# Kernel tuning notes

Hardware: AMD Instinct MI355X
Metric: run time of the kernel (lower is better)

## Reference

```python
import jax, jax.numpy as jnp
import numpy as np


def setup_inputs() -> dict:
    key = jax.random.key(0)
    k1, k2 = jax.random.split(key)
    B, C, N = 8, 3, 4096
    ori_pcs = jax.random.normal(k1, (B, C, N), dtype=jnp.float32)
    adv_pcs = jax.random.normal(k2, (B, C, N), dtype=jnp.float32)
    return {"ori_pcs": ori_pcs, "adv_pcs": adv_pcs}


def _chamfer(ori_pcs, adv_pcs, single=False, reduce="max"):
    # [B, 3, N] -> [B, N, 3]
    x = jnp.swapaxes(ori_pcs, 1, 2)
    y = jnp.swapaxes(adv_pcs, 1, 2)
    x2 = jnp.sum(x * x, axis=-1)  # [B, N]
    y2 = jnp.sum(y * y, axis=-1)  # [B, M]
    # squared pairwise distances [B, N, M]
    d = x2[:, :, None] + y2[:, None, :] - 2.0 * jnp.einsum("bnd,bmd->bnm", x, y)
    d = jnp.maximum(d, 0.0)
    d1 = jnp.mean(jnp.min(d, axis=2), axis=1)  # ori -> adv, per batch [B]
    if single:
        return jnp.mean(d1)
    d2 = jnp.mean(jnp.min(d, axis=1), axis=1)  # adv -> ori, per batch [B]
    if reduce == "max":
        per_batch = jnp.maximum(d1, d2)
    else:  # 'sum' / 'mean' style fallback
        per_batch = d1 + d2
    return jnp.mean(per_batch)


def reference(ori_pcs, adv_pcs):
    return _chamfer(ori_pcs, adv_pcs, single=False, reduce="max")
```

## Files before the change

### kernel.cpp

```cpp
#include <hip/hip_runtime.h>
#include <float.h>

#define BATCH 8
#define NPTS 4096
#define BLK 512
#define THALF 1024
#define NH 4
#define NRG 8

typedef __attribute__((ext_vector_type(8))) short short8;
typedef __attribute__((ext_vector_type(16))) float floatx16;

union U4S8 { uint4 u; short8 s; };

__device__ inline unsigned short f2bf(float f) {
    unsigned u = __float_as_uint(f);
    return (unsigned short)((u + 0x7FFFu + ((u >> 16) & 1u)) >> 16);
}
__device__ inline float bf2f(unsigned short h) {
    return __uint_as_float(((unsigned)h) << 16);
}
__device__ inline unsigned flag_token(int i) {
    return 0x9E3779B9u * (unsigned)(i + 7);
}

__global__ __launch_bounds__(BLK, 4) void chamfer_partial(
        const float* __restrict__ ori, const float* __restrict__ adv,
        float* __restrict__ rfin) {
    __shared__ uint4 sm[THALF];

    int bx = blockIdx.x;
    int half = bx & (NH - 1);
    int rowgroup = (bx >> 2) & (NRG - 1);
    int dirb = bx >> 5;
    int b = dirb & 7;
    int dir = dirb >> 3;

    const float* qsrc = dir ? adv : ori;
    const float* tsrc = dir ? ori : adv;

    {
        const float* tx = tsrc + (b * 3 + 0) * NPTS;
        const float* ty = tsrc + (b * 3 + 1) * NPTS;
        const float* tz = tsrc + (b * 3 + 2) * NPTS;
        #pragma unroll
        for (int i = 0; i < THALF / BLK; ++i) {
            int p = threadIdx.x + i * BLK;
            int m = half * THALF + p;
            float x = tx[m], y = ty[m], z = tz[m];
            float n2 = fmaf(x, x, fmaf(y, y, z * z));
            unsigned short hx = f2bf(x), hy = f2bf(y), hz = f2bf(z);
            unsigned short lx = f2bf(x - bf2f(hx));
            unsigned short ly = f2bf(y - bf2f(hy));
            unsigned short lz = f2bf(z - bf2f(hz));
            unsigned short h2 = f2bf(n2);
            unsigned short l2 = f2bf(n2 - bf2f(h2));
            uint4 u;
            u.x = (unsigned)hx | ((unsigned)hy << 16);
            u.y = (unsigned)hz | ((unsigned)lx << 16);
            u.z = (unsigned)ly | ((unsigned)lz << 16);
            u.w = (unsigned)h2 | ((unsigned)l2 << 16);
            sm[p] = u;
        }
    }

    int w = threadIdx.x >> 6;
    int l = threadIdx.x & 63;
    int lrow = l & 31;
    int kh = l >> 5;

    short8 afrag0, afrag1;
    #pragma unroll
    for (int bi = 0; bi < 2; ++bi) {
        int q = rowgroup * 512 + (w * 2 + bi) * 32 + lrow;
        float x = qsrc[(b * 3 + 0) * NPTS + q];
        float y = qsrc[(b * 3 + 1) * NPTS + q];
        float z = qsrc[(b * 3 + 2) * NPTS + q];
        float n2 = fmaf(x, x, fmaf(y, y, z * z));
        unsigned short hx = f2bf(x), hy = f2bf(y), hz = f2bf(z);
        unsigned short lx = f2bf(x - bf2f(hx));
        unsigned short ly = f2bf(y - bf2f(hy));
        unsigned short lz = f2bf(z - bf2f(hz));
        unsigned short h2 = f2bf(n2);
        unsigned short l2 = f2bf(n2 - bf2f(h2));
        unsigned short mhx = f2bf(-2.0f * bf2f(hx));
        unsigned short mhy = f2bf(-2.0f * bf2f(hy));
        unsigned short mhz = f2bf(-2.0f * bf2f(hz));
        unsigned short mlx = f2bf(-2.0f * bf2f(lx));
        unsigned short mly = f2bf(-2.0f * bf2f(ly));
        unsigned short mlz = f2bf(-2.0f * bf2f(lz));
        const unsigned short one = 0x3F80;
        union { unsigned short us[8]; short8 s8; } A;
        if (kh == 0) {
            A.us[0] = mhx; A.us[1] = mhy; A.us[2] = mhz;
            A.us[3] = mhx; A.us[4] = mhy; A.us[5] = mhz;
            A.us[6] = one; A.us[7] = one;
        } else {
            A.us[0] = mlx; A.us[1] = mly; A.us[2] = mlz;
            A.us[3] = h2;  A.us[4] = l2;
            A.us[5] = 0;   A.us[6] = 0;   A.us[7] = 0;
        }
        if (bi == 0) afrag0 = A.s8; else afrag1 = A.s8;
    }
    __syncthreads();

    floatx16 zero, rmn0, rmn1;
    #pragma unroll
    for (int r = 0; r < 16; ++r) { zero[r] = 0.0f; rmn0[r] = FLT_MAX; rmn1[r] = FLT_MAX; }

    bool hi = (kh == 1);
    int col = lrow;

    {
        uint4 r0 = sm[col], r1 = sm[32 + col];
        #pragma unroll 1
        for (int ct = 0; ct < 32; ct += 2) {
            U4S8 f0, f1;
            f0.u.x = r0.x;
            f0.u.y = hi ? ((r0.y & 0xFFFFu) | 0x3F800000u) : r0.y;
            f0.u.z = hi ? 0x00003F80u : r0.z;
            f0.u.w = hi ? 0u : r0.w;
            f1.u.x = r1.x;
            f1.u.y = hi ? ((r1.y & 0xFFFFu) | 0x3F800000u) : r1.y;
            f1.u.z = hi ? 0x00003F80u : r1.z;
            f1.u.w = hi ? 0u : r1.w;
            int nt = (ct + 2) & 31;
            r0 = sm[(nt << 5) + col];
            r1 = sm[((nt + 1) << 5) + col];
            {
                floatx16 a0 = __builtin_amdgcn_mfma_f32_32x32x16_bf16(afrag0, f0.s, zero, 0, 0, 0);
                floatx16 a1 = __builtin_amdgcn_mfma_f32_32x32x16_bf16(afrag0, f1.s, zero, 0, 0, 0);
                #pragma unroll
                for (int r = 0; r < 16; ++r)
                    rmn0[r] = fminf(fminf(rmn0[r], a0[r]), a1[r]);
            }
            {
                floatx16 c0 = __builtin_amdgcn_mfma_f32_32x32x16_bf16(afrag1, f0.s, zero, 0, 0, 0);
                floatx16 c1 = __builtin_amdgcn_mfma_f32_32x32x16_bf16(afrag1, f1.s, zero, 0, 0, 0);
                #pragma unroll
                for (int r = 0; r < 16; ++r)
                    rmn1[r] = fminf(fminf(rmn1[r], c0[r]), c1[r]);
            }
        }
    }

    bool b0 = (l & 1), b1 = (l & 2), b2 = (l & 4), b3 = (l & 8);

#define FOLD(v)                                                                \
    {                                                                          \
        _Pragma("unroll")                                                      \
        for (int i = 0; i < 8; ++i) {                                          \
            float send = b0 ? v[i] : v[i + 8];                                 \
            float recv = __shfl_xor(send, 1);                                  \
            v[i] = fminf(b0 ? v[i + 8] : v[i], recv);                          \
        }                                                                      \
        _Pragma("unroll")                                                      \
        for (int i = 0; i < 4; ++i) {                                          \
            float send = b1 ? v[i] : v[i + 4];                                 \
            float recv = __shfl_xor(send, 2);                                  \
            v[i] = fminf(b1 ? v[i + 4] : v[i], recv);                          \
        }                                                                      \
        _Pragma("unroll")                                                      \
        for (int i = 0; i < 2; ++i) {                                          \
            float send = b2 ? v[i] : v[i + 2];                                 \
            float recv = __shfl_xor(send, 4);                                  \
            v[i] = fminf(b2 ? v[i + 2] : v[i], recv);                          \
        }                                                                      \
        {                                                                      \
            float send = b3 ? v[0] : v[1];                                     \
            float recv = __shfl_xor(send, 8);                                  \
            v[0] = fminf(b3 ? v[1] : v[0], recv);                              \
        }                                                                      \
        v[0] = fminf(v[0], __shfl_xor(v[0], 16));                              \
    }

    FOLD(rmn0);
    FOLD(rmn1);
#undef FOLD

    if ((l & 16) == 0) {
        int g = l & 15;
        int rr = ((g & 1) << 3) | ((g & 2) << 1) | ((g & 4) >> 1) | ((g & 8) >> 3);
        int rowin = (rr & 3) + 8 * (rr >> 2) + 4 * kh;
        float* base = rfin + (((size_t)(dirb * NH + half)) << 12)
                    + rowgroup * 512;
        base[(w * 2 + 0) * 32 + rowin] = rmn0[0];
        base[(w * 2 + 1) * 32 + rowin] = rmn1[0];
    }
}

__global__ __launch_bounds__(256) void combine_kernel(
        const float* __restrict__ rfin, float* __restrict__ bsum,
        unsigned* __restrict__ flags, float* __restrict__ out) {
    __shared__ float ws[4];
    __shared__ float sh[16];
    int dirb = blockIdx.x;
    const float* p = rfin + (((size_t)dirb * NH) << 12);
    float s = 0.0f;
    #pragma unroll
    for (int k = 0; k < 16; ++k) {
        int row = k * 256 + threadIdx.x;
        float m = fminf(fminf(p[row], p[(1 << 12) + row]),
                        fminf(p[(2 << 12) + row], p[(3 << 12) + row]));
        s += fmaxf(m, 0.0f);
    }
    for (int off = 32; off > 0; off >>= 1) s += __shfl_down(s, off);
    int wid = threadIdx.x >> 6, lane = threadIdx.x & 63;
    if (lane == 0) ws[wid] = s;
    __syncthreads();
    if (threadIdx.x == 0) {
        float t = ws[0] + ws[1] + ws[2] + ws[3];
        atomicExch((unsigned*)(bsum + dirb), __float_as_uint(t));
        __threadfence();
        atomicExch(flags + dirb, flag_token(dirb));
    }

    if (dirb == 0) {
        __syncthreads();
        int t = threadIdx.x;
        if (t < 16) {
            unsigned want = flag_token(t);
            while (atomicAdd(flags + t, 0u) != want) {
                __builtin_amdgcn_s_sleep(1);
            }
            sh[t] = __uint_as_float(atomicAdd((unsigned*)(bsum + t), 0u));
        }
        __syncthreads();
        if (t == 0) {
            float acc = 0.0f;
            #pragma unroll
            for (int bb = 0; bb < BATCH; ++bb)
                acc += fmaxf(sh[bb], sh[8 + bb]);
            out[0] = acc * (1.0f / (float)NPTS) * (1.0f / (float)BATCH);
        }
    }
}

extern "C" void kernel_launch(void* const* d_in, const int* in_sizes, int n_in,
                              void* d_out, int out_size, void* d_ws, size_t ws_size,
                              hipStream_t stream) {
    const float* ori = (const float*)d_in[0];
    const float* adv = (const float*)d_in[1];
    float* out = (float*)d_out;

    float* rfin = (float*)d_ws;
    float* bsum = rfin + (size_t)16 * NH * NPTS;
    unsigned* flags = (unsigned*)(bsum + 16);

    chamfer_partial<<<16 * NRG * NH, BLK, 0, stream>>>(ori, adv, rfin);
    combine_kernel<<<16, 256, 0, stream>>>(rfin, bsum, flags, out);
}
```

Baseline: 19.47 us.

## Precompute B fragments in LDS, software-pipeline MFMA loop, widen combine grid

Stores both the low-half and high-half B fragment variants in shared memory so the inner loop no longer selects and masks fragment words per iteration. The MFMA loop is software-pipelined so one set of min-reductions overlaps the next MFMA pair, with loads issued a step ahead. The combine kernel is split into 64 blocks, each summing a quarter of the rows, and a final block folds the partial sums. This doubles LDS per block and adds more flag spinning in the combine stage.

```diff
diff --git a/kernel.cpp b/kernel.cpp
--- a/kernel.cpp
+++ b/kernel.cpp
@@ -12,6 +12,7 @@
 typedef __attribute__((ext_vector_type(16))) float floatx16;
 
 union U4S8 { uint4 u; short8 s; };
+__device__ inline short8 asS8(uint4 u) { U4S8 t; t.u = u; return t.s; }
 
 __device__ inline unsigned short f2bf(float f) {
     unsigned u = __float_as_uint(f);
@@ -27,7 +28,7 @@
 __global__ __launch_bounds__(BLK, 4) void chamfer_partial(
         const float* __restrict__ ori, const float* __restrict__ adv,
         float* __restrict__ rfin) {
-    __shared__ uint4 sm[THALF];
+    __shared__ uint4 fr[2 * THALF];
 
     int bx = blockIdx.x;
     int half = bx & (NH - 1);
@@ -55,12 +56,18 @@
             unsigned short lz = f2bf(z - bf2f(hz));
             unsigned short h2 = f2bf(n2);
             unsigned short l2 = f2bf(n2 - bf2f(h2));
-            uint4 u;
-            u.x = (unsigned)hx | ((unsigned)hy << 16);
-            u.y = (unsigned)hz | ((unsigned)lx << 16);
-            u.z = (unsigned)ly | ((unsigned)lz << 16);
-            u.w = (unsigned)h2 | ((unsigned)l2 << 16);
-            sm[p] = u;
+            uint4 v0;
+            v0.x = (unsigned)hx | ((unsigned)hy << 16);
+            v0.y = (unsigned)hz | ((unsigned)lx << 16);
+            v0.z = (unsigned)ly | ((unsigned)lz << 16);
+            v0.w = (unsigned)h2 | ((unsigned)l2 << 16);
+            uint4 v1;
+            v1.x = v0.x;
+            v1.y = (unsigned)hz | (0x3F80u << 16);
+            v1.z = 0x00003F80u;
+            v1.w = 0u;
+            fr[p] = v0;
+            fr[THALF + p] = v1;
         }
     }
 
@@ -108,40 +115,39 @@
     #pragma unroll
     for (int r = 0; r < 16; ++r) { zero[r] = 0.0f; rmn0[r] = FLT_MAX; rmn1[r] = FLT_MAX; }
 
-    bool hi = (kh == 1);
-    int col = lrow;
+    const uint4* tp = fr + kh * THALF + lrow;
 
     {
-        uint4 r0 = sm[col], r1 = sm[32 + col];
+        uint4 f0 = tp[0], f1 = tp[1 << 5];
+        floatx16 a0 = __builtin_amdgcn_mfma_f32_32x32x16_bf16(afrag0, asS8(f0), zero, 0, 0, 0);
+        floatx16 a1 = __builtin_amdgcn_mfma_f32_32x32x16_bf16(afrag0, asS8(f1), zero, 0, 0, 0);
+        uint4 fn0 = tp[2 << 5], fn1 = tp[3 << 5];
+        #pragma unroll
+        for (int r = 0; r < 16; ++r)
+            rmn0[r] = fminf(fminf(rmn0[r], a0[r]), a1[r]);
+        floatx16 c0 = __builtin_amdgcn_mfma_f32_32x32x16_bf16(afrag1, asS8(f0), zero, 0, 0, 0);
+        floatx16 c1 = __builtin_amdgcn_mfma_f32_32x32x16_bf16(afrag1, asS8(f1), zero, 0, 0, 0);
+        f0 = fn0; f1 = fn1;
+
         #pragma unroll 1
-        for (int ct = 0; ct < 32; ct += 2) {
-            U4S8 f0, f1;
-            f0.u.x = r0.x;
-            f0.u.y = hi ? ((r0.y & 0xFFFFu) | 0x3F800000u) : r0.y;
-            f0.u.z = hi ? 0x00003F80u : r0.z;
-            f0.u.w = hi ? 0u : r0.w;
-            f1.u.x = r1.x;
-            f1.u.y = hi ? ((r1.y & 0xFFFFu) | 0x3F800000u) : r1.y;
-            f1.u.z = hi ? 0x00003F80u : r1.z;
-            f1.u.w = hi ? 0u : r1.w;
+        for (int ct = 2; ct < 32; ct += 2) {
+            #pragma unroll
+            for (int r = 0; r < 16; ++r)
+                rmn1[r] = fminf(fminf(rmn1[r], c0[r]), c1[r]);
+            a0 = __builtin_amdgcn_mfma_f32_32x32x16_bf16(afrag0, asS8(f0), zero, 0, 0, 0);
+            a1 = __builtin_amdgcn_mfma_f32_32x32x16_bf16(afrag0, asS8(f1), zero, 0, 0, 0);
             int nt = (ct + 2) & 31;
-            r0 = sm[(nt << 5) + col];
-            r1 = sm[((nt + 1) << 5) + col];
-            {
-                floatx16 a0 = __builtin_amdgcn_mfma_f32_32x32x16_bf16(afrag0, f0.s, zero, 0, 0, 0);
-                floatx16 a1 = __builtin_amdgcn_mfma_f32_32x32x16_bf16(afrag0, f1.s, zero, 0, 0, 0);
-                #pragma unroll
-                for (int r = 0; r < 16; ++r)
-                    rmn0[r] = fminf(fminf(rmn0[r], a0[r]), a1[r]);
-            }
-            {
-                floatx16 c0 = __builtin_amdgcn_mfma_f32_32x32x16_bf16(afrag1, f0.s, zero, 0, 0, 0);
-                floatx16 c1 = __builtin_amdgcn_mfma_f32_32x32x16_bf16(afrag1, f1.s, zero, 0, 0, 0);
-                #pragma unroll
-                for (int r = 0; r < 16; ++r)
-                    rmn1[r] = fminf(fminf(rmn1[r], c0[r]), c1[r]);
-            }
-        }
+            fn0 = tp[nt << 5]; fn1 = tp[(nt + 1) << 5];
+            #pragma unroll
+            for (int r = 0; r < 16; ++r)
+                rmn0[r] = fminf(fminf(rmn0[r], a0[r]), a1[r]);
+            c0 = __builtin_amdgcn_mfma_f32_32x32x16_bf16(afrag1, asS8(f0), zero, 0, 0, 0);
+            c1 = __builtin_amdgcn_mfma_f32_32x32x16_bf16(afrag1, asS8(f1), zero, 0, 0, 0);
+            f0 = fn0; f1 = fn1;
+        }
+        #pragma unroll
+        for (int r = 0; r < 16; ++r)
+            rmn1[r] = fminf(fminf(rmn1[r], c0[r]), c1[r]);
     }
 
     bool b0 = (l & 1), b1 = (l & 2), b2 = (l & 4), b3 = (l & 8);
@@ -190,16 +196,17 @@
 }
 
 __global__ __launch_bounds__(256) void combine_kernel(
-        const float* __restrict__ rfin, float* __restrict__ bsum,
+        const float* __restrict__ rfin, float* __restrict__ pb,
         unsigned* __restrict__ flags, float* __restrict__ out) {
     __shared__ float ws[4];
-    __shared__ float sh[16];
-    int dirb = blockIdx.x;
+    __shared__ float sh[64 + 16];
+    int cb = blockIdx.x;
+    int dirb = cb >> 2, slice = cb & 3;
     const float* p = rfin + (((size_t)dirb * NH) << 12);
     float s = 0.0f;
     #pragma unroll
-    for (int k = 0; k < 16; ++k) {
-        int row = k * 256 + threadIdx.x;
+    for (int k = 0; k < 4; ++k) {
+        int row = slice * 1024 + k * 256 + threadIdx.x;
         float m = fminf(fminf(p[row], p[(1 << 12) + row]),
                         fminf(p[(2 << 12) + row], p[(3 << 12) + row]));
         s += fmaxf(m, 0.0f);
@@ -210,27 +217,31 @@
     __syncthreads();
     if (threadIdx.x == 0) {
         float t = ws[0] + ws[1] + ws[2] + ws[3];
-        atomicExch((unsigned*)(bsum + dirb), __float_as_uint(t));
+        atomicExch((unsigned*)(pb + cb), __float_as_uint(t));
         __threadfence();
-        atomicExch(flags + dirb, flag_token(dirb));
-    }
-
-    if (dirb == 0) {
+        atomicExch(flags + cb, flag_token(cb));
+    }
+
+    if (cb == 0) {
         __syncthreads();
         int t = threadIdx.x;
-        if (t < 16) {
+        if (t < 64) {
             unsigned want = flag_token(t);
             while (atomicAdd(flags + t, 0u) != want) {
                 __builtin_amdgcn_s_sleep(1);
             }
-            sh[t] = __uint_as_float(atomicAdd((unsigned*)(bsum + t), 0u));
+            sh[t] = __uint_as_float(atomicAdd((unsigned*)(pb + t), 0u));
+        }
+        __syncthreads();
+        if (t < 16) {
+            sh[64 + t] = sh[t * 4] + sh[t * 4 + 1] + sh[t * 4 + 2] + sh[t * 4 + 3];
         }
         __syncthreads();
         if (t == 0) {
             float acc = 0.0f;
             #pragma unroll
             for (int bb = 0; bb < BATCH; ++bb)
-                acc += fmaxf(sh[bb], sh[8 + bb]);
+                acc += fmaxf(sh[64 + bb], sh[64 + 8 + bb]);
             out[0] = acc * (1.0f / (float)NPTS) * (1.0f / (float)BATCH);
         }
     }
@@ -244,9 +255,9 @@
     float* out = (float*)d_out;
 
     float* rfin = (float*)d_ws;
-    float* bsum = rfin + (size_t)16 * NH * NPTS;
-    unsigned* flags = (unsigned*)(bsum + 16);
+    float* pb = rfin + (size_t)16 * NH * NPTS;
+    unsigned* flags = (unsigned*)(pb + 64);
 
     chamfer_partial<<<16 * NRG * NH, BLK, 0, stream>>>(ori, adv, rfin);
-    combine_kernel<<<16, 256, 0, stream>>>(rfin, bsum, flags, out);
-}
+    combine_kernel<<<64, 256, 0, stream>>>(rfin, pb, flags, out);
+}
```

Measured after the change: 19.00 us. 1.02x faster.

## Shrink partial blocks to one query tile per wave and widen combine grid

Applied to the files above, without the earlier changes.

The main kernel drops from 512 to 256 threads per block, and each wave now handles a single 32-row query tile instead of two. The row-group count rises from 8 to 32, so the grid goes from 512 to 2048 blocks, and the MFMA issue is moved ahead of the next LDS prefetch. The combine kernel is split into 64 blocks, each reducing a quarter of a direction-batch's rows, with a final two-level sum in block 0. The goal is more parallelism and occupancy on the many-CU GPU. The cost is that each block restages the same 1024-point target tile to LDS for half the MFMA work, and block 0 now spin-waits on 64 flags instead of 16.

```diff
diff --git a/kernel.cpp b/kernel.cpp
--- a/kernel.cpp
+++ b/kernel.cpp
@@ -3,15 +3,16 @@
 
 #define BATCH 8
 #define NPTS 4096
-#define BLK 512
+#define BLK 256
 #define THALF 1024
 #define NH 4
-#define NRG 8
+#define NRG 32
 
 typedef __attribute__((ext_vector_type(8))) short short8;
 typedef __attribute__((ext_vector_type(16))) float floatx16;
 
 union U4S8 { uint4 u; short8 s; };
+__device__ inline short8 asS8(uint4 u) { U4S8 t; t.u = u; return t.s; }
 
 __device__ inline unsigned short f2bf(float f) {
     unsigned u = __float_as_uint(f);
@@ -24,7 +25,7 @@
     return 0x9E3779B9u * (unsigned)(i + 7);
 }
 
-__global__ __launch_bounds__(BLK, 4) void chamfer_partial(
+__global__ __launch_bounds__(BLK, 6) void chamfer_partial(
         const float* __restrict__ ori, const float* __restrict__ adv,
         float* __restrict__ rfin) {
     __shared__ uint4 sm[THALF];
@@ -32,7 +33,7 @@
     int bx = blockIdx.x;
     int half = bx & (NH - 1);
     int rowgroup = (bx >> 2) & (NRG - 1);
-    int dirb = bx >> 5;
+    int dirb = bx >> 7;
     int b = dirb & 7;
     int dir = dirb >> 3;
 
@@ -69,10 +70,9 @@
     int lrow = l & 31;
     int kh = l >> 5;
 
-    short8 afrag0, afrag1;
-    #pragma unroll
-    for (int bi = 0; bi < 2; ++bi) {
-        int q = rowgroup * 512 + (w * 2 + bi) * 32 + lrow;
+    short8 afrag;
+    {
+        int q = rowgroup * 128 + w * 32 + lrow;
         float x = qsrc[(b * 3 + 0) * NPTS + q];
         float y = qsrc[(b * 3 + 1) * NPTS + q];
         float z = qsrc[(b * 3 + 2) * NPTS + q];
@@ -100,13 +100,13 @@
             A.us[3] = h2;  A.us[4] = l2;
             A.us[5] = 0;   A.us[6] = 0;   A.us[7] = 0;
         }
-        if (bi == 0) afrag0 = A.s8; else afrag1 = A.s8;
+        afrag = A.s8;
     }
     __syncthreads();
 
-    floatx16 zero, rmn0, rmn1;
+    floatx16 zero, rmn;
     #pragma unroll
-    for (int r = 0; r < 16; ++r) { zero[r] = 0.0f; rmn0[r] = FLT_MAX; rmn1[r] = FLT_MAX; }
+    for (int r = 0; r < 16; ++r) { zero[r] = 0.0f; rmn[r] = FLT_MAX; }
 
     bool hi = (kh == 1);
     int col = lrow;
@@ -124,82 +124,67 @@
             f1.u.y = hi ? ((r1.y & 0xFFFFu) | 0x3F800000u) : r1.y;
             f1.u.z = hi ? 0x00003F80u : r1.z;
             f1.u.w = hi ? 0u : r1.w;
+            floatx16 a0 = __builtin_amdgcn_mfma_f32_32x32x16_bf16(afrag, f0.s, zero, 0, 0, 0);
+            floatx16 a1 = __builtin_amdgcn_mfma_f32_32x32x16_bf16(afrag, f1.s, zero, 0, 0, 0);
             int nt = (ct + 2) & 31;
             r0 = sm[(nt << 5) + col];
             r1 = sm[((nt + 1) << 5) + col];
-            {
-                floatx16 a0 = __builtin_amdgcn_mfma_f32_32x32x16_bf16(afrag0, f0.s, zero, 0, 0, 0);
-                floatx16 a1 = __builtin_amdgcn_mfma_f32_32x32x16_bf16(afrag0, f1.s, zero, 0, 0, 0);
-                #pragma unroll
-                for (int r = 0; r < 16; ++r)
-                    rmn0[r] = fminf(fminf(rmn0[r], a0[r]), a1[r]);
-            }
-            {
-                floatx16 c0 = __builtin_amdgcn_mfma_f32_32x32x16_bf16(afrag1, f0.s, zero, 0, 0, 0);
-                floatx16 c1 = __builtin_amdgcn_mfma_f32_32x32x16_bf16(afrag1, f1.s, zero, 0, 0, 0);
-                #pragma unroll
-                for (int r = 0; r < 16; ++r)
-                    rmn1[r] = fminf(fminf(rmn1[r], c0[r]), c1[r]);
-            }
+            #pragma unroll
+            for (int r = 0; r < 16; ++r)
+                rmn[r] = fminf(fminf(rmn[r], a0[r]), a1[r]);
         }
     }
 
     bool b0 = (l & 1), b1 = (l & 2), b2 = (l & 4), b3 = (l & 8);
-
-#define FOLD(v)                                                                \
-    {                                                                          \
-        _Pragma("unroll")                                                      \
-        for (int i = 0; i < 8; ++i) {                                          \
-            float send = b0 ? v[i] : v[i + 8];                                 \
-            float recv = __shfl_xor(send, 1);                                  \
-            v[i] = fminf(b0 ? v[i + 8] : v[i], recv);                          \
-        }                                                                      \
-        _Pragma("unroll")                                                      \
-        for (int i = 0; i < 4; ++i) {                                          \
-            float send = b1 ? v[i] : v[i + 4];                                 \
-            float recv = __shfl_xor(send, 2);                                  \
-            v[i] = fminf(b1 ? v[i + 4] : v[i], recv);                          \
-        }                                                                      \
-        _Pragma("unroll")                                                      \
-        for (int i = 0; i < 2; ++i) {                                          \
-            float send = b2 ? v[i] : v[i + 2];                                 \
-            float recv = __shfl_xor(send, 4);                                  \
-            v[i] = fminf(b2 ? v[i + 2] : v[i], recv);                          \
-        }                                                                      \
-        {                                                                      \
-            float send = b3 ? v[0] : v[1];                                     \
-            float recv = __shfl_xor(send, 8);                                  \
-            v[0] = fminf(b3 ? v[1] : v[0], recv);                              \
-        }                                                                      \
-        v[0] = fminf(v[0], __shfl_xor(v[0], 16));                              \
-    }
-
-    FOLD(rmn0);
-    FOLD(rmn1);
-#undef FOLD
+    {
+        #pragma unroll
+        for (int i = 0; i < 8; ++i) {
+            float send = b0 ? rmn[i] : rmn[i + 8];
+            float recv = __shfl_xor(send, 1);
+            rmn[i] = fminf(b0 ? rmn[i + 8] : rmn[i], recv);
+        }
+        #pragma unroll
+        for (int i = 0; i < 4; ++i) {
+            float send = b1 ? rmn[i] : rmn[i + 4];
+            float recv = __shfl_xor(send, 2);
+            rmn[i] = fminf(b1 ? rmn[i + 4] : rmn[i], recv);
+        }
+        #pragma unroll
+        for (int i = 0; i < 2; ++i) {
+            float send = b2 ? rmn[i] : rmn[i + 2];
+            float recv = __shfl_xor(send, 4);
+            rmn[i] = fminf(b2 ? rmn[i + 2] : rmn[i], recv);
+        }
+        {
+            float send = b3 ? rmn[0] : rmn[1];
+            float recv = __shfl_xor(send, 8);
+            rmn[0] = fminf(b3 ? rmn[1] : rmn[0], recv);
+        }
+        rmn[0] = fminf(rmn[0], __shfl_xor(rmn[0], 16));
+    }
 
     if ((l & 16) == 0) {
         int g = l & 15;
         int rr = ((g & 1) << 3) | ((g & 2) << 1) | ((g & 4) >> 1) | ((g & 8) >> 3);
         int rowin = (rr & 3) + 8 * (rr >> 2) + 4 * kh;
         float* base = rfin + (((size_t)(dirb * NH + half)) << 12)
-                    + rowgroup * 512;
-        base[(w * 2 + 0) * 32 + rowin] = rmn0[0];
-        base[(w * 2 + 1) * 32 + rowin] = rmn1[0];
+                    + rowgroup * 128;
+        base[w * 32 + rowin] = rmn[0];
     }
 }
 
 __global__ __launch_bounds__(256) void combine_kernel(
-        const float* __restrict__ rfin, float* __restrict__ bsum,
+        const float* __restrict__ rfin, float* __restrict__ pb,
         unsigned* __restrict__ flags, float* __restrict__ out) {
     __shared__ float ws[4];
-    __shared__ float sh[16];
-    int dirb = blockIdx.x;
+    __shared__ float sh[64 + 16];
+    int cb = blockIdx.x;
+    int dirb = cb >> 2, slice = cb & 3;
     const float* p = rfin + (((size_t)dirb * NH) << 12);
     float s = 0.0f;
     #pragma unroll
-    for (int k = 0; k < 16; ++k) {
-        int row = k * 256 + threadIdx.x;
+    for (int k = 0; k < 4; ++k) {
+        int row = slice * 1024 + k * 256 + threadIdx.x;
         float m = fminf(fminf(p[row], p[(1 << 12) + row]),
                         fminf(p[(2 << 12) + row], p[(3 << 12) + row]));
         s += fmaxf(m, 0.0f);
@@ -210,27 +195,31 @@
     __syncthreads();
     if (threadIdx.x == 0) {
         float t = ws[0] + ws[1] + ws[2] + ws[3];
-        atomicExch((unsigned*)(bsum + dirb), __float_as_uint(t));
+        atomicExch((unsigned*)(pb + cb), __float_as_uint(t));
         __threadfence();
-        atomicExch(flags + dirb, flag_token(dirb));
-    }
-
-    if (dirb == 0) {
+        atomicExch(flags + cb, flag_token(cb));
+    }
+
+    if (cb == 0) {
         __syncthreads();
         int t = threadIdx.x;
-        if (t < 16) {
+        if (t < 64) {
             unsigned want = flag_token(t);
             while (atomicAdd(flags + t, 0u) != want) {
                 __builtin_amdgcn_s_sleep(1);
             }
-            sh[t] = __uint_as_float(atomicAdd((unsigned*)(bsum + t), 0u));
+            sh[t] = __uint_as_float(atomicAdd((unsigned*)(pb + t), 0u));
+        }
+        __syncthreads();
+        if (t < 16) {
+            sh[64 + t] = sh[t * 4] + sh[t * 4 + 1] + sh[t * 4 + 2] + sh[t * 4 + 3];
         }
         __syncthreads();
         if (t == 0) {
             float acc = 0.0f;
             #pragma unroll
             for (int bb = 0; bb < BATCH; ++bb)
-                acc += fmaxf(sh[bb], sh[8 + bb]);
+                acc += fmaxf(sh[64 + bb], sh[64 + 8 + bb]);
             out[0] = acc * (1.0f / (float)NPTS) * (1.0f / (float)BATCH);
         }
     }
@@ -244,9 +233,9 @@
     float* out = (float*)d_out;
 
     float* rfin = (float*)d_ws;
-    float* bsum = rfin + (size_t)16 * NH * NPTS;
-    unsigned* flags = (unsigned*)(bsum + 16);
+    float* pb = rfin + (size_t)16 * NH * NPTS;
+    unsigned* flags = (unsigned*)(pb + 64);
 
     chamfer_partial<<<16 * NRG * NH, BLK, 0, stream>>>(ori, adv, rfin);
-    combine_kernel<<<16, 256, 0, stream>>>(rfin, bsum, flags, out);
-}
+    combine_kernel<<<64, 256, 0, stream>>>(rfin, pb, flags, out);
+}
```

Result: slower. 21.81 us (+12.0%).
